# Kernel tuning notes

Hardware: AMD Instinct MI355X
Metric: run time of the kernel (lower is better)

Reference implementation:

```python
import jax, jax.numpy as jnp
import numpy as np

B, MSG, H, D, N = 64, 64, 512, 512, 2048


def setup_inputs() -> dict:
    key = jax.random.key(0)
    ks = jax.random.split(key, 20)
    s = 0.02
    return {
        "message": jax.random.normal(ks[0], (B, MSG), jnp.float32),
        "state": jax.random.normal(ks[1], (B, H), jnp.float32),
        "image": jax.random.normal(ks[2], (B, H), jnp.float32),
        "class_descriptors": jax.random.normal(ks[3], (N, D), jnp.float32),
        # GRUCell params (torch layout: gates ordered r, z, n)
        "w_ih": jax.random.normal(ks[4], (3 * H, MSG), jnp.float32) * s,
        "w_hh": jax.random.normal(ks[5], (3 * H, H), jnp.float32) * s,
        "b_ih": jax.random.normal(ks[6], (3 * H,), jnp.float32) * s,
        "b_hh": jax.random.normal(ks[7], (3 * H,), jnp.float32) * s,
        "w_stop": jax.random.normal(ks[8], (1, H), jnp.float32) * s,
        "b_stop": jax.random.normal(ks[9], (1,), jnp.float32) * s,
        "w_y1": jax.random.normal(ks[10], (H, H + D), jnp.float32) * s,
        "b_y1": jax.random.normal(ks[11], (H,), jnp.float32) * s,
        "w_y2": jax.random.normal(ks[12], (1, H), jnp.float32) * s,
        "b_y2": jax.random.normal(ks[13], (1,), jnp.float32) * s,
        "w_state": jax.random.normal(ks[14], (H, H), jnp.float32) * s,
        "b_state": jax.random.normal(ks[15], (H,), jnp.float32) * s,
        "w_desc": jax.random.normal(ks[16], (H, D), jnp.float32) * s,  # no bias
        "w_msg": jax.random.normal(ks[17], (MSG, H), jnp.float32) * s,
        "b_msg": jax.random.normal(ks[18], (MSG,), jnp.float32) * s,
    }


def _gru_cell(x, h, w_ih, w_hh, b_ih, b_hh):
    gi = x @ w_ih.T + b_ih  # [B, 3H]
    gh = h @ w_hh.T + b_hh
    i_r, i_z, i_n = jnp.split(gi, 3, axis=1)
    h_r, h_z, h_n = jnp.split(gh, 3, axis=1)
    r = jax.nn.sigmoid(i_r + h_r)
    z = jax.nn.sigmoid(i_z + h_z)
    n = jnp.tanh(i_n + r * h_n)
    return (1.0 - z) * n + z * h


def reference(message, state, image, class_descriptors,
              w_ih, w_hh, b_ih, b_hh, w_stop, b_stop,
              w_y1, b_y1, w_y2, b_y2, w_state, b_state,
              w_desc, w_msg, b_msg):
    b, h = state.shape
    n, d = class_descriptors.shape

    new_state = _gru_cell(message, state, w_ih, w_hh, b_ih, b_hh)  # [B, H]
    stop_dist = jax.nn.sigmoid(new_state @ w_stop.T + b_stop)  # [B, 1]
    stop_bit = jax.lax.stop_gradient(jnp.round(stop_dist))  # eval-mode path

    # build_state_descriptor_pairs (faithful to torch view semantics,
    # including the (B, H, N) -> (B*N, H) interleaved reshape of pair_left)
    pair_left = jnp.broadcast_to(new_state[:, :, None], (b, h, n)).reshape(b * n, h)
    pair_right = jnp.broadcast_to(class_descriptors[None], (b, n, d)).reshape(b * n, d)
    pairs = jnp.concatenate([pair_left, pair_right], axis=1)  # [B*N, H+D]

    y = jnp.clip(pairs @ w_y1.T + b_y1, 0.0, None)  # relu, [B*N, H]
    y = (y @ w_y2.T + b_y2).reshape(b, -1)  # [B, N]
    y_scores = jax.lax.stop_gradient(jax.nn.softmax(y, axis=1))

    # reweight_descriptors: softmax-weighted sum over descriptors
    descriptor_influence = jnp.einsum('bn,nd->bd', y_scores, class_descriptors)

    message_state = jnp.tanh(new_state @ w_state.T + b_state
                             + descriptor_influence @ w_desc.T)
    message_dist = jax.nn.sigmoid(message_state @ w_msg.T + b_msg)  # [B, MSG]
    outp_msg = jax.lax.stop_gradient(jnp.round(message_dist))

    return stop_bit, stop_dist, outp_msg, message_dist, y
```

## Files before the change

kernel.cpp:

```cpp
#include <hip/hip_runtime.h>


__device__ __forceinline__ float sigm(float x) { return 1.0f / (1.0f + expf(-x)); }

__device__ __forceinline__ void stage_pad68(float* dst, const float* src, int c) {
  *(float4*)&dst[(c >> 4) * 68 + (c & 15) * 4] = *(const float4*)&src[c * 4];
}

__global__ __launch_bounds__(512) void gruws1_kernel(
    const float* __restrict__ msg, const float* __restrict__ st,
    const float* __restrict__ w_ih, const float* __restrict__ w_hh,
    const float* __restrict__ b_ih, const float* __restrict__ b_hh,
    const float* __restrict__ w_y1,
    float* __restrict__ ns, float* __restrict__ nsT, float* __restrict__ ws1) {
  const int t = threadIdx.x;
  if (blockIdx.x >= 512) {
    const int j = (blockIdx.x - 512) * 8 + (t >> 6);
    const int lane = t & 63;
    const float* row = w_y1 + j * 1024 + lane * 8;
    float4 a = *(const float4*)&row[0];
    float4 b = *(const float4*)&row[4];
    float acc = a.x + a.y + a.z + a.w + b.x + b.y + b.z + b.w;
    #pragma unroll
    for (int m = 1; m < 64; m <<= 1) acc += __shfl_xor(acc, m, 64);
    if (lane == 0) ws1[j] = acc;
    return;
  }
  const int h = blockIdx.x;
  __shared__ __align__(16) float sHr[544], sHz[544], sHn[544];
  __shared__ __align__(16) float sIr[64], sIz[64], sIn[64];
  if (t < 128)      stage_pad68(sHr, w_hh + h * 512, t);
  else if (t < 256) stage_pad68(sHz, w_hh + (h + 512) * 512, t - 128);
  else if (t < 384) stage_pad68(sHn, w_hh + (h + 1024) * 512, t - 256);
  else if (t < 400) ((float4*)sIr)[t - 384] = ((const float4*)(w_ih + h * 64))[t - 384];
  else if (t < 416) ((float4*)sIz)[t - 400] = ((const float4*)(w_ih + (h + 512) * 64))[t - 400];
  else if (t < 432) ((float4*)sIn)[t - 416] = ((const float4*)(w_ih + (h + 1024) * 64))[t - 416];
  __syncthreads();
  const int bi = t >> 3, kg = t & 7;
  float pr = 0.f, pz = 0.f, pin = 0.f, phn = 0.f;
  {
    const float* mrow = msg + bi * 64 + kg * 8;
    const float* ir = &sIr[kg * 8];
    const float* iz = &sIz[kg * 8];
    const float* in_ = &sIn[kg * 8];
    #pragma unroll
    for (int i = 0; i < 2; ++i) {
      float4 x = *(const float4*)&mrow[i * 4];
      float4 wr = *(const float4*)&ir[i * 4];
      float4 wz = *(const float4*)&iz[i * 4];
      float4 wn = *(const float4*)&in_[i * 4];
      pr = fmaf(x.x, wr.x, pr); pr = fmaf(x.y, wr.y, pr); pr = fmaf(x.z, wr.z, pr); pr = fmaf(x.w, wr.w, pr);
      pz = fmaf(x.x, wz.x, pz); pz = fmaf(x.y, wz.y, pz); pz = fmaf(x.z, wz.z, pz); pz = fmaf(x.w, wz.w, pz);
      pin = fmaf(x.x, wn.x, pin); pin = fmaf(x.y, wn.y, pin); pin = fmaf(x.z, wn.z, pin); pin = fmaf(x.w, wn.w, pin);
    }
  }
  {
    const float* srow = st + bi * 512 + kg * 64;
    const float* hr = &sHr[kg * 68];
    const float* hz = &sHz[kg * 68];
    const float* hn = &sHn[kg * 68];
    #pragma unroll
    for (int i = 0; i < 16; ++i) {
      float4 x = *(const float4*)&srow[i * 4];
      float4 wr = *(const float4*)&hr[i * 4];
      float4 wz = *(const float4*)&hz[i * 4];
      float4 wn = *(const float4*)&hn[i * 4];
      pr = fmaf(x.x, wr.x, pr); pr = fmaf(x.y, wr.y, pr); pr = fmaf(x.z, wr.z, pr); pr = fmaf(x.w, wr.w, pr);
      pz = fmaf(x.x, wz.x, pz); pz = fmaf(x.y, wz.y, pz); pz = fmaf(x.z, wz.z, pz); pz = fmaf(x.w, wz.w, pz);
      phn = fmaf(x.x, wn.x, phn); phn = fmaf(x.y, wn.y, phn); phn = fmaf(x.z, wn.z, phn); phn = fmaf(x.w, wn.w, phn);
    }
  }
  pr += __shfl_xor(pr, 1, 8); pr += __shfl_xor(pr, 2, 8); pr += __shfl_xor(pr, 4, 8);
  pz += __shfl_xor(pz, 1, 8); pz += __shfl_xor(pz, 2, 8); pz += __shfl_xor(pz, 4, 8);
  pin += __shfl_xor(pin, 1, 8); pin += __shfl_xor(pin, 2, 8); pin += __shfl_xor(pin, 4, 8);
  phn += __shfl_xor(phn, 1, 8); phn += __shfl_xor(phn, 2, 8); phn += __shfl_xor(phn, 4, 8);
  if ((t & 7) == 0) {
    float r = sigm(pr + b_ih[h] + b_hh[h]);
    float z = sigm(pz + b_ih[h + 512] + b_hh[h + 512]);
    float n = tanhf(pin + b_ih[h + 1024] + r * (phn + b_hh[h + 1024]));
    float hp = st[bi * 512 + h];
    float v = (1.0f - z) * n + z * hp;
    ns[bi * 512 + h] = v;
    nsT[h * 64 + bi] = v;
  }
}

__global__ __launch_bounds__(256, 2) void g_kernel(
    const float* __restrict__ desc, const float* __restrict__ w_y1,
    const float* __restrict__ b_y1, float* __restrict__ G) {
  __shared__ __align__(16) float As[32 * 33];
  __shared__ __align__(16) float Bs[32 * 68];
  const int rr0 = blockIdx.x * 32;
  const int j0 = blockIdx.y * 64;
  const int t = threadIdx.x;
  const int lrow = t >> 3;
  const int lk4 = (t & 7) * 4;
  const int tm2 = (t >> 4) * 2;
  const int tn4 = (t & 15) * 4;
  const float* aptr = desc + (rr0 + lrow) * 512 + lk4;
  const float* bptr0 = w_y1 + (j0 + lrow) * 1024 + 512 + lk4;
  const float* bptr1 = bptr0 + 32 * 1024;
  float4 av = *(const float4*)aptr;
  float4 bv0 = *(const float4*)bptr0;
  float4 bv1 = *(const float4*)bptr1;
  float acc[2][4] = {};
  for (int k0 = 0; k0 < 512; k0 += 32) {
    __syncthreads();
    As[(lk4 + 0) * 33 + lrow] = av.x; As[(lk4 + 1) * 33 + lrow] = av.y;
    As[(lk4 + 2) * 33 + lrow] = av.z; As[(lk4 + 3) * 33 + lrow] = av.w;
    Bs[(lk4 + 0) * 68 + lrow] = bv0.x; Bs[(lk4 + 1) * 68 + lrow] = bv0.y;
    Bs[(lk4 + 2) * 68 + lrow] = bv0.z; Bs[(lk4 + 3) * 68 + lrow] = bv0.w;
    Bs[(lk4 + 0) * 68 + lrow + 32] = bv1.x; Bs[(lk4 + 1) * 68 + lrow + 32] = bv1.y;
    Bs[(lk4 + 2) * 68 + lrow + 32] = bv1.z; Bs[(lk4 + 3) * 68 + lrow + 32] = bv1.w;
    __syncthreads();
    if (k0 + 32 < 512) {
      av = *(const float4*)(aptr + k0 + 32);
      bv0 = *(const float4*)(bptr0 + k0 + 32);
      bv1 = *(const float4*)(bptr1 + k0 + 32);
    }
    #pragma unroll
    for (int k = 0; k < 32; ++k) {
      float a0 = As[k * 33 + tm2];
      float a1 = As[k * 33 + tm2 + 1];
      float4 b = *(const float4*)&Bs[k * 68 + tn4];
      acc[0][0] = fmaf(a0, b.x, acc[0][0]); acc[0][1] = fmaf(a0, b.y, acc[0][1]);
      acc[0][2] = fmaf(a0, b.z, acc[0][2]); acc[0][3] = fmaf(a0, b.w, acc[0][3]);
      acc[1][0] = fmaf(a1, b.x, acc[1][0]); acc[1][1] = fmaf(a1, b.y, acc[1][1]);
      acc[1][2] = fmaf(a1, b.z, acc[1][2]); acc[1][3] = fmaf(a1, b.w, acc[1][3]);
    }
  }
  float4 by = *(const float4*)&b_y1[j0 + tn4];
  float4 r0 = make_float4(acc[0][0] + by.x, acc[0][1] + by.y, acc[0][2] + by.z, acc[0][3] + by.w);
  float4 r1 = make_float4(acc[1][0] + by.x, acc[1][1] + by.y, acc[1][2] + by.z, acc[1][3] + by.w);
  *(float4*)&G[(rr0 + tm2) * 512 + j0 + tn4] = r0;
  *(float4*)&G[(rr0 + tm2 + 1) * 512 + j0 + tn4] = r1;
}

__global__ __launch_bounds__(256) void ystop_kernel(
    const float* __restrict__ nsT, const float* __restrict__ ws1,
    const float* __restrict__ G, const float* __restrict__ w_y2,
    const float* __restrict__ b_y2, float* __restrict__ yf,
    const float* __restrict__ ns, const float* __restrict__ w_stop,
    const float* __restrict__ b_stop, float* __restrict__ out_bit,
    float* __restrict__ out_dist) {
  const int t = threadIdx.x;
  if (blockIdx.x == 2048) {
    const int bi = t >> 2, kg = t & 3;
    const float* row = ns + bi * 512 + kg * 128;
    const float* wrow = w_stop + kg * 128;
    float acc = 0.f;
    #pragma unroll
    for (int i = 0; i < 32; ++i) {
      float4 r = *(const float4*)&row[i * 4];
      float4 w = *(const float4*)&wrow[i * 4];
      acc = fmaf(r.x, w.x, acc); acc = fmaf(r.y, w.y, acc);
      acc = fmaf(r.z, w.z, acc); acc = fmaf(r.w, w.w, acc);
    }
    acc += __shfl_xor(acc, 1, 4); acc += __shfl_xor(acc, 2, 4);
    if (kg == 0) {
      float sd = sigm(acc + b_stop[0]);
      out_dist[bi] = sd;
      out_bit[bi] = rintf(sd);
    }
    return;
  }
  const int rr = blockIdx.x;
  __shared__ __align__(16) float sG[512], sW1[512], sW2[512];
  __shared__ float sp[4 * 72];
  if (t < 128) {
    ((float4*)sG)[t] = ((const float4*)(G + rr * 512))[t];
    ((float4*)sW2)[t] = ((const float4*)w_y2)[t];
  } else {
    ((float4*)sW1)[t - 128] = ((const float4*)ws1)[t - 128];
  }
  __syncthreads();
  const int bi = t & 63, jq = t >> 6;
  const float v = nsT[(rr >> 2) * 64 + bi];
  float acc = 0.0f;
  const float* g = sG + jq * 128;
  const float* w1 = sW1 + jq * 128;
  const float* w2 = sW2 + jq * 128;
  #pragma unroll 4
  for (int j = 0; j < 128; j += 4) {
    float4 gv = *(const float4*)&g[j];
    float4 a1 = *(const float4*)&w1[j];
    float4 a2 = *(const float4*)&w2[j];
    acc = fmaf(a2.x, fmaxf(fmaf(v, a1.x, gv.x), 0.0f), acc);
    acc = fmaf(a2.y, fmaxf(fmaf(v, a1.y, gv.y), 0.0f), acc);
    acc = fmaf(a2.z, fmaxf(fmaf(v, a1.z, gv.z), 0.0f), acc);
    acc = fmaf(a2.w, fmaxf(fmaf(v, a1.w, gv.w), 0.0f), acc);
  }
  sp[jq * 72 + bi] = acc;
  __syncthreads();
  if (t < 64) {
    float y = sp[t] + sp[72 + t] + sp[144 + t] + sp[216 + t] + b_y2[0];
    yf[t * 2048 + rr] = y;
  }
}

__global__ __launch_bounds__(256) void softmax_kernel(
    const float* __restrict__ yf, float* __restrict__ scores,
    float* __restrict__ out_y) {
  const int bi = blockIdx.x;
  const int t = threadIdx.x;
  __shared__ float sy[2048];
  __shared__ float red[256];
  float lmax = -3.0e38f;
  for (int i = t; i < 2048; i += 256) {
    float v = yf[bi * 2048 + i];
    sy[i] = v;
    out_y[bi * 2048 + i] = v;
    lmax = fmaxf(lmax, v);
  }
  red[t] = lmax;
  __syncthreads();
  for (int s = 128; s > 0; s >>= 1) {
    if (t < s) red[t] = fmaxf(red[t], red[t + s]);
    __syncthreads();
  }
  const float mx = red[0];
  __syncthreads();
  float lsum = 0.0f;
  for (int i = t; i < 2048; i += 256) {
    float e = expf(sy[i] - mx);
    sy[i] = e;
    lsum += e;
  }
  red[t] = lsum;
  __syncthreads();
  for (int s = 128; s > 0; s >>= 1) {
    if (t < s) red[t] += red[t + s];
    __syncthreads();
  }
  const float inv = 1.0f / red[0];
  for (int i = t; i < 2048; i += 256) scores[bi * 2048 + i] = sy[i] * inv;
}

__global__ __launch_bounds__(256) void di_part_kernel(
    const float* __restrict__ scores, const float* __restrict__ desc,
    float* __restrict__ dp) {
  __shared__ __align__(16) float sS[64][64];
  __shared__ __align__(16) float sD[64][64];
  const int d0 = blockIdx.x * 64;
  const int n0 = blockIdx.y * 64;
  const int tid = threadIdx.x;
  {
    const int bi = tid >> 2;
    #pragma unroll
    for (int i = 0; i < 4; ++i) {
      const int kq = (tid & 3) * 4 + i * 16;
      float4 av = *(const float4*)&scores[bi * 2048 + n0 + kq];
      sS[kq + 0][bi] = av.x; sS[kq + 1][bi] = av.y;
      sS[kq + 2][bi] = av.z; sS[kq + 3][bi] = av.w;
    }
  }
  {
    #pragma unroll
    for (int i = 0; i < 4; ++i) {
      const int nn = (tid >> 4) + i * 16;
      const int dq = (tid & 15) * 4;
      *(float4*)&sD[nn][dq] = *(const float4*)&desc[(n0 + nn) * 512 + d0 + dq];
    }
  }
  __syncthreads();
  const int bi0 = (tid >> 4) * 4;
  const int dd0 = (tid & 15) * 4;
  float acc[4][4] = {};
  #pragma unroll 8
  for (int nn = 0; nn < 64; ++nn) {
    float4 a = *(const float4*)&sS[nn][bi0];
    float4 b = *(const float4*)&sD[nn][dd0];
    acc[0][0] = fmaf(a.x, b.x, acc[0][0]); acc[0][1] = fmaf(a.x, b.y, acc[0][1]);
    acc[0][2] = fmaf(a.x, b.z, acc[0][2]); acc[0][3] = fmaf(a.x, b.w, acc[0][3]);
    acc[1][0] = fmaf(a.y, b.x, acc[1][0]); acc[1][1] = fmaf(a.y, b.y, acc[1][1]);
    acc[1][2] = fmaf(a.y, b.z, acc[1][2]); acc[1][3] = fmaf(a.y, b.w, acc[1][3]);
    acc[2][0] = fmaf(a.z, b.x, acc[2][0]); acc[2][1] = fmaf(a.z, b.y, acc[2][1]);
    acc[2][2] = fmaf(a.z, b.z, acc[2][2]); acc[2][3] = fmaf(a.z, b.w, acc[2][3]);
    acc[3][0] = fmaf(a.w, b.x, acc[3][0]); acc[3][1] = fmaf(a.w, b.y, acc[3][1]);
    acc[3][2] = fmaf(a.w, b.z, acc[3][2]); acc[3][3] = fmaf(a.w, b.w, acc[3][3]);
  }
  float* base = dp + blockIdx.y * 32768;
  #pragma unroll
  for (int i = 0; i < 4; ++i)
    #pragma unroll
    for (int j = 0; j < 4; ++j)
      base[(bi0 + i) * 512 + d0 + dd0 + j] = acc[i][j];
}

__global__ __launch_bounds__(512) void di_reduce_kernel(
    const float* __restrict__ dp, float* __restrict__ di) {
  const int idx = blockIdx.x * 512 + threadIdx.x;
  float acc = 0.0f;
  #pragma unroll 8
  for (int c = 0; c < 32; ++c) acc += dp[c * 32768 + idx];
  di[idx] = acc;
}

__global__ __launch_bounds__(512) void ms_kernel(
    const float* __restrict__ ns, const float* __restrict__ di,
    const float* __restrict__ w_state, const float* __restrict__ b_state,
    const float* __restrict__ w_desc, float* __restrict__ ms) {
  const int hj = blockIdx.x;
  const int t = threadIdx.x;
  __shared__ __align__(16) float sWs[544], sWd[544];
  if (t < 128)      stage_pad68(sWs, w_state + hj * 512, t);
  else if (t < 256) stage_pad68(sWd, w_desc + hj * 512, t - 128);
  __syncthreads();
  const int bi = t >> 3, kg = t & 7;
  const float* nr = ns + bi * 512 + kg * 64;
  const float* dr = di + bi * 512 + kg * 64;
  const float* wsp = &sWs[kg * 68];
  const float* wdp = &sWd[kg * 68];
  float acc = 0.f;
  #pragma unroll
  for (int i = 0; i < 16; ++i) {
    float4 a = *(const float4*)&nr[i * 4];
    float4 w = *(const float4*)&wsp[i * 4];
    float4 b = *(const float4*)&dr[i * 4];
    float4 u = *(const float4*)&wdp[i * 4];
    acc = fmaf(a.x, w.x, acc); acc = fmaf(a.y, w.y, acc);
    acc = fmaf(a.z, w.z, acc); acc = fmaf(a.w, w.w, acc);
    acc = fmaf(b.x, u.x, acc); acc = fmaf(b.y, u.y, acc);
    acc = fmaf(b.z, u.z, acc); acc = fmaf(b.w, u.w, acc);
  }
  acc += __shfl_xor(acc, 1, 8); acc += __shfl_xor(acc, 2, 8); acc += __shfl_xor(acc, 4, 8);
  if ((t & 7) == 0) ms[bi * 512 + hj] = tanhf(acc + b_state[hj]);
}

__global__ __launch_bounds__(512) void msg_kernel(
    const float* __restrict__ ms, const float* __restrict__ w_msg,
    const float* __restrict__ b_msg, float* __restrict__ out_msg,
    float* __restrict__ out_msgdist) {
  const int m = blockIdx.x;
  const int t = threadIdx.x;
  __shared__ __align__(16) float sW[544];
  if (t < 128) stage_pad68(sW, w_msg + m * 512, t);
  __syncthreads();
  const int bi = t >> 3, kg = t & 7;
  const float* row = ms + bi * 512 + kg * 64;
  const float* wp = &sW[kg * 68];
  float acc = 0.f;
  #pragma unroll
  for (int i = 0; i < 16; ++i) {
    float4 a = *(const float4*)&row[i * 4];
    float4 w = *(const float4*)&wp[i * 4];
    acc = fmaf(a.x, w.x, acc); acc = fmaf(a.y, w.y, acc);
    acc = fmaf(a.z, w.z, acc); acc = fmaf(a.w, w.w, acc);
  }
  acc += __shfl_xor(acc, 1, 8); acc += __shfl_xor(acc, 2, 8); acc += __shfl_xor(acc, 4, 8);
  if ((t & 7) == 0) {
    float md = sigm(acc + b_msg[m]);
    out_msgdist[bi * 64 + m] = md;
    out_msg[bi * 64 + m] = rintf(md);
  }
}

extern "C" void kernel_launch(void* const* d_in, const int* in_sizes, int n_in,
                              void* d_out, int out_size, void* d_ws, size_t ws_size,
                              hipStream_t stream) {
  (void)in_sizes; (void)n_in; (void)out_size; (void)ws_size;
  const float* message = (const float*)d_in[0];
  const float* state   = (const float*)d_in[1];
  const float* desc    = (const float*)d_in[3];
  const float* w_ih    = (const float*)d_in[4];
  const float* w_hh    = (const float*)d_in[5];
  const float* b_ih    = (const float*)d_in[6];
  const float* b_hh    = (const float*)d_in[7];
  const float* w_stop  = (const float*)d_in[8];
  const float* b_stop  = (const float*)d_in[9];
  const float* w_y1    = (const float*)d_in[10];
  const float* b_y1    = (const float*)d_in[11];
  const float* w_y2    = (const float*)d_in[12];
  const float* b_y2    = (const float*)d_in[13];
  const float* w_state = (const float*)d_in[14];
  const float* b_state = (const float*)d_in[15];
  const float* w_desc  = (const float*)d_in[16];
  const float* w_msg   = (const float*)d_in[17];
  const float* b_msg   = (const float*)d_in[18];

  float* out = (float*)d_out;
  float* out_stopbit  = out;
  float* out_stopdist = out + 64;
  float* out_msg      = out + 128;
  float* out_msgdist  = out + 4224;
  float* out_y        = out + 8320;

  char* ws = (char*)d_ws;
  float* ns     = (float*)(ws);
  float* nsT    = (float*)(ws + 131072);
  float* ws1    = (float*)(ws + 262144);
  float* G      = (float*)(ws + 264192);
  float* yf     = (float*)(ws + 4458496);
  float* scores = (float*)(ws + 4982784);
  float* di     = (float*)(ws + 5507072);
  float* ms     = (float*)(ws + 5638144);

  gruws1_kernel<<<576, 512, 0, stream>>>(message, state, w_ih, w_hh, b_ih, b_hh,
                                         w_y1, ns, nsT, ws1);
  g_kernel<<<dim3(64, 8), 256, 0, stream>>>(desc, w_y1, b_y1, G);
  ystop_kernel<<<2049, 256, 0, stream>>>(nsT, ws1, G, w_y2, b_y2, yf,
                                         ns, w_stop, b_stop, out_stopbit, out_stopdist);
  softmax_kernel<<<64, 256, 0, stream>>>(yf, scores, out_y);
  di_part_kernel<<<dim3(8, 32), 256, 0, stream>>>(scores, desc, G);
  di_reduce_kernel<<<64, 512, 0, stream>>>(G, di);
  ms_kernel<<<512, 512, 0, stream>>>(ns, di, w_state, b_state, w_desc, ms);
  msg_kernel<<<64, 512, 0, stream>>>(ms, w_msg, b_msg, out_msg, out_msgdist);
}
```

Measured before the change: 194.6 us.

## Fuse GEMM into GRU launch, defer softmax normalization, atomically reduce descriptor influence

```diff
diff --git a/kernel.cpp b/kernel.cpp
--- a/kernel.cpp
+++ b/kernel.cpp
@@ -7,15 +7,64 @@
   *(float4*)&dst[(c >> 4) * 68 + (c & 15) * 4] = *(const float4*)&src[c * 4];
 }
 
-__global__ __launch_bounds__(512) void gruws1_kernel(
+__global__ __launch_bounds__(512) void a_kernel(
     const float* __restrict__ msg, const float* __restrict__ st,
     const float* __restrict__ w_ih, const float* __restrict__ w_hh,
     const float* __restrict__ b_ih, const float* __restrict__ b_hh,
-    const float* __restrict__ w_y1,
-    float* __restrict__ ns, float* __restrict__ nsT, float* __restrict__ ws1) {
-  const int t = threadIdx.x;
-  if (blockIdx.x >= 512) {
-    const int j = (blockIdx.x - 512) * 8 + (t >> 6);
+    const float* __restrict__ w_y1, const float* __restrict__ b_y1,
+    const float* __restrict__ desc,
+    float* __restrict__ ns, float* __restrict__ nsT, float* __restrict__ ws1,
+    float* __restrict__ G) {
+  __shared__ __align__(16) float sm[4352];
+  const int t = threadIdx.x;
+  const int blk = blockIdx.x;
+
+  if (blk >= 576) {
+    const int q = blk - 576;
+    const int rr0 = (q >> 3) * 64;
+    const int j0 = (q & 7) * 64;
+    float* As = sm;
+    float* Bs = sm + 2176;
+    const int lrow = t >> 3;
+    const int lk4 = (t & 7) * 4;
+    const int tm2 = (t >> 4) * 2;
+    const int tn4 = (t & 15) * 4;
+    const float* aptr = desc + (rr0 + lrow) * 512 + lk4;
+    const float* bptr = w_y1 + (j0 + lrow) * 1024 + 512 + lk4;
+    float4 av = *(const float4*)aptr;
+    float4 bv = *(const float4*)bptr;
+    float acc[2][4] = {};
+    for (int k0 = 0; k0 < 512; k0 += 32) {
+      __syncthreads();
+      As[(lk4 + 0) * 68 + lrow] = av.x; As[(lk4 + 1) * 68 + lrow] = av.y;
+      As[(lk4 + 2) * 68 + lrow] = av.z; As[(lk4 + 3) * 68 + lrow] = av.w;
+      Bs[(lk4 + 0) * 68 + lrow] = bv.x; Bs[(lk4 + 1) * 68 + lrow] = bv.y;
+      Bs[(lk4 + 2) * 68 + lrow] = bv.z; Bs[(lk4 + 3) * 68 + lrow] = bv.w;
+      __syncthreads();
+      if (k0 + 32 < 512) {
+        av = *(const float4*)(aptr + k0 + 32);
+        bv = *(const float4*)(bptr + k0 + 32);
+      }
+      #pragma unroll
+      for (int k = 0; k < 32; ++k) {
+        float2 a = *(const float2*)&As[k * 68 + tm2];
+        float4 b = *(const float4*)&Bs[k * 68 + tn4];
+        acc[0][0] = fmaf(a.x, b.x, acc[0][0]); acc[0][1] = fmaf(a.x, b.y, acc[0][1]);
+        acc[0][2] = fmaf(a.x, b.z, acc[0][2]); acc[0][3] = fmaf(a.x, b.w, acc[0][3]);
+        acc[1][0] = fmaf(a.y, b.x, acc[1][0]); acc[1][1] = fmaf(a.y, b.y, acc[1][1]);
+        acc[1][2] = fmaf(a.y, b.z, acc[1][2]); acc[1][3] = fmaf(a.y, b.w, acc[1][3]);
+      }
+    }
+    float4 by = *(const float4*)&b_y1[j0 + tn4];
+    float4 r0 = make_float4(acc[0][0] + by.x, acc[0][1] + by.y, acc[0][2] + by.z, acc[0][3] + by.w);
+    float4 r1 = make_float4(acc[1][0] + by.x, acc[1][1] + by.y, acc[1][2] + by.z, acc[1][3] + by.w);
+    *(float4*)&G[(rr0 + tm2) * 512 + j0 + tn4] = r0;
+    *(float4*)&G[(rr0 + tm2 + 1) * 512 + j0 + tn4] = r1;
+    return;
+  }
+
+  if (blk >= 512) {
+    const int j = (blk - 512) * 8 + (t >> 6);
     const int lane = t & 63;
     const float* row = w_y1 + j * 1024 + lane * 8;
     float4 a = *(const float4*)&row[0];
@@ -26,9 +75,14 @@
     if (lane == 0) ws1[j] = acc;
     return;
   }
-  const int h = blockIdx.x;
-  __shared__ __align__(16) float sHr[544], sHz[544], sHn[544];
-  __shared__ __align__(16) float sIr[64], sIz[64], sIn[64];
+
+  const int h = blk;
+  float* sHr = sm;
+  float* sHz = sm + 544;
+  float* sHn = sm + 1088;
+  float* sIr = sm + 1632;
+  float* sIz = sm + 1696;
+  float* sIn = sm + 1760;
   if (t < 128)      stage_pad68(sHr, w_hh + h * 512, t);
   else if (t < 256) stage_pad68(sHz, w_hh + (h + 512) * 512, t - 128);
   else if (t < 384) stage_pad68(sHn, w_hh + (h + 1024) * 512, t - 256);
@@ -85,65 +139,19 @@
   }
 }
 
-__global__ __launch_bounds__(256, 2) void g_kernel(
-    const float* __restrict__ desc, const float* __restrict__ w_y1,
-    const float* __restrict__ b_y1, float* __restrict__ G) {
-  __shared__ __align__(16) float As[32 * 33];
-  __shared__ __align__(16) float Bs[32 * 68];
-  const int rr0 = blockIdx.x * 32;
-  const int j0 = blockIdx.y * 64;
-  const int t = threadIdx.x;
-  const int lrow = t >> 3;
-  const int lk4 = (t & 7) * 4;
-  const int tm2 = (t >> 4) * 2;
-  const int tn4 = (t & 15) * 4;
-  const float* aptr = desc + (rr0 + lrow) * 512 + lk4;
-  const float* bptr0 = w_y1 + (j0 + lrow) * 1024 + 512 + lk4;
-  const float* bptr1 = bptr0 + 32 * 1024;
-  float4 av = *(const float4*)aptr;
-  float4 bv0 = *(const float4*)bptr0;
-  float4 bv1 = *(const float4*)bptr1;
-  float acc[2][4] = {};
-  for (int k0 = 0; k0 < 512; k0 += 32) {
-    __syncthreads();
-    As[(lk4 + 0) * 33 + lrow] = av.x; As[(lk4 + 1) * 33 + lrow] = av.y;
-    As[(lk4 + 2) * 33 + lrow] = av.z; As[(lk4 + 3) * 33 + lrow] = av.w;
-    Bs[(lk4 + 0) * 68 + lrow] = bv0.x; Bs[(lk4 + 1) * 68 + lrow] = bv0.y;
-    Bs[(lk4 + 2) * 68 + lrow] = bv0.z; Bs[(lk4 + 3) * 68 + lrow] = bv0.w;
-    Bs[(lk4 + 0) * 68 + lrow + 32] = bv1.x; Bs[(lk4 + 1) * 68 + lrow + 32] = bv1.y;
-    Bs[(lk4 + 2) * 68 + lrow + 32] = bv1.z; Bs[(lk4 + 3) * 68 + lrow + 32] = bv1.w;
-    __syncthreads();
-    if (k0 + 32 < 512) {
-      av = *(const float4*)(aptr + k0 + 32);
-      bv0 = *(const float4*)(bptr0 + k0 + 32);
-      bv1 = *(const float4*)(bptr1 + k0 + 32);
-    }
-    #pragma unroll
-    for (int k = 0; k < 32; ++k) {
-      float a0 = As[k * 33 + tm2];
-      float a1 = As[k * 33 + tm2 + 1];
-      float4 b = *(const float4*)&Bs[k * 68 + tn4];
-      acc[0][0] = fmaf(a0, b.x, acc[0][0]); acc[0][1] = fmaf(a0, b.y, acc[0][1]);
-      acc[0][2] = fmaf(a0, b.z, acc[0][2]); acc[0][3] = fmaf(a0, b.w, acc[0][3]);
-      acc[1][0] = fmaf(a1, b.x, acc[1][0]); acc[1][1] = fmaf(a1, b.y, acc[1][1]);
-      acc[1][2] = fmaf(a1, b.z, acc[1][2]); acc[1][3] = fmaf(a1, b.w, acc[1][3]);
-    }
-  }
-  float4 by = *(const float4*)&b_y1[j0 + tn4];
-  float4 r0 = make_float4(acc[0][0] + by.x, acc[0][1] + by.y, acc[0][2] + by.z, acc[0][3] + by.w);
-  float4 r1 = make_float4(acc[1][0] + by.x, acc[1][1] + by.y, acc[1][2] + by.z, acc[1][3] + by.w);
-  *(float4*)&G[(rr0 + tm2) * 512 + j0 + tn4] = r0;
-  *(float4*)&G[(rr0 + tm2 + 1) * 512 + j0 + tn4] = r1;
-}
-
 __global__ __launch_bounds__(256) void ystop_kernel(
     const float* __restrict__ nsT, const float* __restrict__ ws1,
     const float* __restrict__ G, const float* __restrict__ w_y2,
     const float* __restrict__ b_y2, float* __restrict__ yf,
     const float* __restrict__ ns, const float* __restrict__ w_stop,
     const float* __restrict__ b_stop, float* __restrict__ out_bit,
-    float* __restrict__ out_dist) {
-  const int t = threadIdx.x;
+    float* __restrict__ out_dist, float* __restrict__ di) {
+  const int t = threadIdx.x;
+  if (blockIdx.x > 2048) {
+    const int idx = (blockIdx.x - 2049) * 512 + t * 2;
+    *(float2*)&di[idx] = make_float2(0.f, 0.f);
+    return;
+  }
   if (blockIdx.x == 2048) {
     const int bi = t >> 2, kg = t & 3;
     const float* row = ns + bi * 512 + kg * 128;
@@ -199,8 +207,8 @@
 }
 
 __global__ __launch_bounds__(256) void softmax_kernel(
-    const float* __restrict__ yf, float* __restrict__ scores,
-    float* __restrict__ out_y) {
+    const float* __restrict__ yf, float* __restrict__ out_y,
+    float* __restrict__ mxv, float* __restrict__ sumv) {
   const int bi = blockIdx.x;
   const int t = threadIdx.x;
   __shared__ float sy[2048];
@@ -221,55 +229,54 @@
   const float mx = red[0];
   __syncthreads();
   float lsum = 0.0f;
-  for (int i = t; i < 2048; i += 256) {
-    float e = expf(sy[i] - mx);
-    sy[i] = e;
-    lsum += e;
-  }
+  for (int i = t; i < 2048; i += 256) lsum += expf(sy[i] - mx);
   red[t] = lsum;
   __syncthreads();
   for (int s = 128; s > 0; s >>= 1) {
     if (t < s) red[t] += red[t + s];
     __syncthreads();
   }
-  const float inv = 1.0f / red[0];
-  for (int i = t; i < 2048; i += 256) scores[bi * 2048 + i] = sy[i] * inv;
+  if (t == 0) { mxv[bi] = mx; sumv[bi] = red[0]; }
 }
 
 __global__ __launch_bounds__(256) void di_part_kernel(
-    const float* __restrict__ scores, const float* __restrict__ desc,
-    float* __restrict__ dp) {
-  __shared__ __align__(16) float sS[64][64];
-  __shared__ __align__(16) float sD[64][64];
+    const float* __restrict__ yf, const float* __restrict__ mxv,
+    const float* __restrict__ desc, float* __restrict__ di) {
+  __shared__ __align__(16) float sE[64 * 66];
+  __shared__ __align__(16) float sD[64 * 68];
+  __shared__ float sMx[64];
   const int d0 = blockIdx.x * 64;
   const int n0 = blockIdx.y * 64;
-  const int tid = threadIdx.x;
+  const int t = threadIdx.x;
+  if (t < 64) sMx[t] = mxv[t];
+  __syncthreads();
   {
-    const int bi = tid >> 2;
+    const int bi = t >> 2;
+    const float m = sMx[bi];
     #pragma unroll
     for (int i = 0; i < 4; ++i) {
-      const int kq = (tid & 3) * 4 + i * 16;
-      float4 av = *(const float4*)&scores[bi * 2048 + n0 + kq];
-      sS[kq + 0][bi] = av.x; sS[kq + 1][bi] = av.y;
-      sS[kq + 2][bi] = av.z; sS[kq + 3][bi] = av.w;
-    }
-  }
-  {
+      const int kq = (t & 3) * 4 + i * 16;
+      float4 av = *(const float4*)&yf[bi * 2048 + n0 + kq];
+      sE[(kq + 0) * 66 + bi] = expf(av.x - m);
+      sE[(kq + 1) * 66 + bi] = expf(av.y - m);
+      sE[(kq + 2) * 66 + bi] = expf(av.z - m);
+      sE[(kq + 3) * 66 + bi] = expf(av.w - m);
+    }
     #pragma unroll
     for (int i = 0; i < 4; ++i) {
-      const int nn = (tid >> 4) + i * 16;
-      const int dq = (tid & 15) * 4;
-      *(float4*)&sD[nn][dq] = *(const float4*)&desc[(n0 + nn) * 512 + d0 + dq];
-    }
-  }
-  __syncthreads();
-  const int bi0 = (tid >> 4) * 4;
-  const int dd0 = (tid & 15) * 4;
+      const int nn = (t >> 4) + i * 16;
+      const int dq = (t & 15) * 4;
+      *(float4*)&sD[nn * 68 + dq] = *(const float4*)&desc[(n0 + nn) * 512 + d0 + dq];
+    }
+  }
+  __syncthreads();
+  const int bi0 = (t >> 4) * 4;
+  const int dd0 = (t & 15) * 4;
   float acc[4][4] = {};
   #pragma unroll 8
   for (int nn = 0; nn < 64; ++nn) {
-    float4 a = *(const float4*)&sS[nn][bi0];
-    float4 b = *(const float4*)&sD[nn][dd0];
+    float4 a = *(const float4*)&sE[nn * 66 + bi0];
+    float4 b = *(const float4*)&sD[nn * 68 + dd0];
     acc[0][0] = fmaf(a.x, b.x, acc[0][0]); acc[0][1] = fmaf(a.x, b.y, acc[0][1]);
     acc[0][2] = fmaf(a.x, b.z, acc[0][2]); acc[0][3] = fmaf(a.x, b.w, acc[0][3]);
     acc[1][0] = fmaf(a.y, b.x, acc[1][0]); acc[1][1] = fmaf(a.y, b.y, acc[1][1]);
@@ -279,52 +286,47 @@
     acc[3][0] = fmaf(a.w, b.x, acc[3][0]); acc[3][1] = fmaf(a.w, b.y, acc[3][1]);
     acc[3][2] = fmaf(a.w, b.z, acc[3][2]); acc[3][3] = fmaf(a.w, b.w, acc[3][3]);
   }
-  float* base = dp + blockIdx.y * 32768;
   #pragma unroll
   for (int i = 0; i < 4; ++i)
     #pragma unroll
     for (int j = 0; j < 4; ++j)
-      base[(bi0 + i) * 512 + d0 + dd0 + j] = acc[i][j];
-}
-
-__global__ __launch_bounds__(512) void di_reduce_kernel(
-    const float* __restrict__ dp, float* __restrict__ di) {
-  const int idx = blockIdx.x * 512 + threadIdx.x;
-  float acc = 0.0f;
-  #pragma unroll 8
-  for (int c = 0; c < 32; ++c) acc += dp[c * 32768 + idx];
-  di[idx] = acc;
+      atomicAdd(&di[(bi0 + i) * 512 + d0 + dd0 + j], acc[i][j]);
 }
 
 __global__ __launch_bounds__(512) void ms_kernel(
     const float* __restrict__ ns, const float* __restrict__ di,
+    const float* __restrict__ sumv,
     const float* __restrict__ w_state, const float* __restrict__ b_state,
     const float* __restrict__ w_desc, float* __restrict__ ms) {
   const int hj = blockIdx.x;
   const int t = threadIdx.x;
   __shared__ __align__(16) float sWs[544], sWd[544];
+  __shared__ float sInv[64];
   if (t < 128)      stage_pad68(sWs, w_state + hj * 512, t);
   else if (t < 256) stage_pad68(sWd, w_desc + hj * 512, t - 128);
+  else if (t < 320) sInv[t - 256] = 1.0f / sumv[t - 256];
   __syncthreads();
   const int bi = t >> 3, kg = t & 7;
   const float* nr = ns + bi * 512 + kg * 64;
   const float* dr = di + bi * 512 + kg * 64;
   const float* wsp = &sWs[kg * 68];
   const float* wdp = &sWd[kg * 68];
-  float acc = 0.f;
+  float accs = 0.f, accd = 0.f;
   #pragma unroll
   for (int i = 0; i < 16; ++i) {
     float4 a = *(const float4*)&nr[i * 4];
     float4 w = *(const float4*)&wsp[i * 4];
     float4 b = *(const float4*)&dr[i * 4];
     float4 u = *(const float4*)&wdp[i * 4];
-    acc = fmaf(a.x, w.x, acc); acc = fmaf(a.y, w.y, acc);
-    acc = fmaf(a.z, w.z, acc); acc = fmaf(a.w, w.w, acc);
-    acc = fmaf(b.x, u.x, acc); acc = fmaf(b.y, u.y, acc);
-    acc = fmaf(b.z, u.z, acc); acc = fmaf(b.w, u.w, acc);
-  }
-  acc += __shfl_xor(acc, 1, 8); acc += __shfl_xor(acc, 2, 8); acc += __shfl_xor(acc, 4, 8);
-  if ((t & 7) == 0) ms[bi * 512 + hj] = tanhf(acc + b_state[hj]);
+    accs = fmaf(a.x, w.x, accs); accs = fmaf(a.y, w.y, accs);
+    accs = fmaf(a.z, w.z, accs); accs = fmaf(a.w, w.w, accs);
+    accd = fmaf(b.x, u.x, accd); accd = fmaf(b.y, u.y, accd);
+    accd = fmaf(b.z, u.z, accd); accd = fmaf(b.w, u.w, accd);
+  }
+  accs += __shfl_xor(accs, 1, 8); accs += __shfl_xor(accs, 2, 8); accs += __shfl_xor(accs, 4, 8);
+  accd += __shfl_xor(accd, 1, 8); accd += __shfl_xor(accd, 2, 8); accd += __shfl_xor(accd, 4, 8);
+  if ((t & 7) == 0)
+    ms[bi * 512 + hj] = tanhf(accs + accd * sInv[bi] + b_state[hj]);
 }
 
 __global__ __launch_bounds__(512) void msg_kernel(
@@ -386,23 +388,23 @@
   float* out_y        = out + 8320;
 
   char* ws = (char*)d_ws;
-  float* ns     = (float*)(ws);
-  float* nsT    = (float*)(ws + 131072);
-  float* ws1    = (float*)(ws + 262144);
-  float* G      = (float*)(ws + 264192);
-  float* yf     = (float*)(ws + 4458496);
-  float* scores = (float*)(ws + 4982784);
-  float* di     = (float*)(ws + 5507072);
-  float* ms     = (float*)(ws + 5638144);
-
-  gruws1_kernel<<<576, 512, 0, stream>>>(message, state, w_ih, w_hh, b_ih, b_hh,
-                                         w_y1, ns, nsT, ws1);
-  g_kernel<<<dim3(64, 8), 256, 0, stream>>>(desc, w_y1, b_y1, G);
-  ystop_kernel<<<2049, 256, 0, stream>>>(nsT, ws1, G, w_y2, b_y2, yf,
-                                         ns, w_stop, b_stop, out_stopbit, out_stopdist);
-  softmax_kernel<<<64, 256, 0, stream>>>(yf, scores, out_y);
-  di_part_kernel<<<dim3(8, 32), 256, 0, stream>>>(scores, desc, G);
-  di_reduce_kernel<<<64, 512, 0, stream>>>(G, di);
-  ms_kernel<<<512, 512, 0, stream>>>(ns, di, w_state, b_state, w_desc, ms);
+  float* ns   = (float*)(ws);
+  float* nsT  = (float*)(ws + 131072);
+  float* ws1  = (float*)(ws + 262144);
+  float* G    = (float*)(ws + 264192);
+  float* yf   = (float*)(ws + 4458496);
+  float* di   = (float*)(ws + 4982784);
+  float* ms   = (float*)(ws + 5113856);
+  float* mxv  = (float*)(ws + 5244928);
+  float* sumv = (float*)(ws + 5245184);
+
+  a_kernel<<<832, 512, 0, stream>>>(message, state, w_ih, w_hh, b_ih, b_hh,
+                                    w_y1, b_y1, desc, ns, nsT, ws1, G);
+  ystop_kernel<<<2113, 256, 0, stream>>>(nsT, ws1, G, w_y2, b_y2, yf,
+                                         ns, w_stop, b_stop, out_stopbit,
+                                         out_stopdist, di);
+  softmax_kernel<<<64, 256, 0, stream>>>(yf, out_y, mxv, sumv);
+  di_part_kernel<<<dim3(8, 32), 256, 0, stream>>>(yf, mxv, desc, di);
+  ms_kernel<<<512, 512, 0, stream>>>(ns, di, sumv, w_state, b_state, w_desc, ms);
   msg_kernel<<<64, 512, 0, stream>>>(ms, w_msg, b_msg, out_msg, out_msgdist);
 }
```

Result: slower. 207.5 us (+6.6%).
